# Kernel tuning notes

Measured on AMD Instinct MI355X. Metric: run time of the kernel, lower is better.

The kernel has to match this reference:

```python
import jax, jax.numpy as jnp
import numpy as np

# ---- Cl(3,0) Cayley table; blade order [1, e1,e2,e3, e12,e13,e23, e123] ----
def _build_cayley():
    blades = [0b000, 0b001, 0b010, 0b100, 0b011, 0b101, 0b110, 0b111]
    pos = {b: i for i, b in enumerate(blades)}
    def sign(a, b):
        s, a = 0, a >> 1
        while a:
            s += bin(a & b).count('1')
            a >>= 1
        return -1.0 if s & 1 else 1.0
    C = np.zeros((8, 8, 8), np.float32)
    for i, a in enumerate(blades):
        for k, b in enumerate(blades):
            C[i, pos[a ^ b], k] = sign(a, b)  # e_a * e_b -> sign * e_(a^b), metric all +1
    return jnp.asarray(C)

CAYLEY = _build_cayley()
EPS = 1e-6
SEQ = 25      # num_nodes (5) + num_edges (20)
HEADS = 8

def _expand_grades(w):
    # [..., 4] (per-grade) -> [..., 8] (per-blade), grade dims 1,3,3,1
    return jnp.concatenate([w[..., 0:1],
                            jnp.repeat(w[..., 1:2], 3, -1),
                            jnp.repeat(w[..., 2:3], 3, -1),
                            w[..., 3:4]], axis=-1)

def mv_linear(x, w, b):
    # x [N, in, 8], w [out, in, 4], b [out]; bias only on scalar blade
    y = jnp.einsum('nmi,omi->noi', x, _expand_grades(w))
    return y.at[..., 0].add(b)

def mv_layernorm(x, a):
    n = jnp.linalg.norm(x, axis=-1, keepdims=True)   # [N, c, 1] multivector norm
    n = jnp.mean(n, axis=1, keepdims=True) + EPS     # mean over channels -> [N, 1, 1]
    return a[None, :, None] * x / n

def mv_silu(x, a, b):
    # invariants: scalar component + squared grade magnitudes (mag2)
    inv = jnp.stack([x[..., 0],
                     jnp.sum(x[..., 1:4] ** 2, -1),
                     jnp.sum(x[..., 4:7] ** 2, -1),
                     x[..., 7] ** 2], axis=-1)       # [N, c, 4]
    return _expand_grades(jax.nn.sigmoid(a * inv + b)) * x

def geometric_product(a, b):
    return jnp.einsum('nci,ijk,nck->ncj', a, CAYLEY, b)


def setup_inputs() -> dict:
    key = jax.random.key(0)
    ks = iter(jax.random.split(key, 40))
    D, B = 128, 1024
    N = B * SEQ
    s = 0.05
    rn = lambda *sh: jax.random.normal(next(ks), sh, jnp.float32) * s
    return dict(
        src=jax.random.normal(next(ks), (N, D, 8), jnp.float32),
        ln1_a=jnp.ones(D, jnp.float32), ln2_a=jnp.ones(D, jnp.float32), ln3_a=jnp.ones(D, jnp.float32),
        wq=rn(D, D, 4), bq=jnp.zeros(D, jnp.float32),
        wk=rn(D, D, 4), bk=jnp.zeros(D, jnp.float32),
        wv=rn(D, D, 4), bv=jnp.zeros(D, jnp.float32),
        wo=rn(D, D, 4), bo=jnp.zeros(D, jnp.float32),
        gw1=rn(2 * D, D, 4), gb1=jnp.zeros(2 * D, jnp.float32),
        gw2=rn(2 * D, D, 4), gb2=jnp.zeros(2 * D, jnp.float32),
        gw3=rn(D, 2 * D, 4), gb3=jnp.zeros(D, jnp.float32),
        gna=jnp.ones(D, jnp.float32),
        mw1=rn(2 * D, D, 4), mb1=jnp.zeros(2 * D, jnp.float32),
        sa=jnp.ones((2 * D, 4), jnp.float32), sb=jnp.zeros((2 * D, 4), jnp.float32),
        mw2=rn(D, 2 * D, 4), mb2=jnp.zeros(D, jnp.float32),
    )


def reference(src, ln1_a, ln2_a, ln3_a, wq, bq, wk, bk, wv, bv, wo, bo,
              gw1, gb1, gw2, gb2, gw3, gb3, gna,
              mw1, mb1, sa, sb, mw2, mb2):
    N, D, _ = src.shape
    B, dh = N // SEQ, D // HEADS

    def attention(x):
        q = mv_linear(x, wq, bq).reshape(B, SEQ, HEADS, dh, 8)
        k = mv_linear(x, wk, bk).reshape(B, SEQ, HEADS, dh, 8)
        v = mv_linear(x, wv, bv).reshape(B, SEQ, HEADS, dh, 8)
        scores = jnp.einsum('bshdi,bthdi->bhst', q, k) / np.float32(np.sqrt(dh * 8))
        p = jax.nn.softmax(scores, axis=-1)
        o = jnp.einsum('bhst,bthdi->bshdi', p, v).reshape(N, D, 8)
        return mv_linear(o, wo, bo)

    # pre-norm attention + residual
    x = src + attention(mv_layernorm(src, ln1_a))
    x = mv_layernorm(x, ln2_a)
    # GP_Layer: two grade-wise linears -> geometric product -> linear -> norm
    xl = mv_linear(x, gw1, gb1)
    xr = mv_linear(x, gw2, gb2)
    g = mv_layernorm(mv_linear(geometric_product(xl, xr), gw3, gb3), gna)
    x = x + g
    x = mv_layernorm(x, ln3_a)
    # gated MLP: MVLinear -> MVSiLU -> MVLinear
    ff = mv_linear(mv_silu(mv_linear(x, mw1, mb1), sa, sb), mw2, mb2)
    return x + ff
```

## Files before the change

kernel.cpp:

```cpp
#include <hip/hip_runtime.h>
#include <hip/hip_bf16.h>
#include <math.h>

#define NROWS 25600
#define SEQL  25
#define EPSV  1e-6f

typedef __hip_bfloat16 bf16;
typedef __attribute__((ext_vector_type(4))) float f32x4;
typedef __attribute__((ext_vector_type(8))) short bf16x8;
typedef __attribute__((ext_vector_type(4))) short s16x4;
typedef unsigned int u32;

#define GLD16(gp_, lp_) __builtin_amdgcn_global_load_lds( \
    (const __attribute__((address_space(1))) u32*)(gp_), \
    (__attribute__((address_space(3))) u32*)(lp_), 16, 0, 0)

__device__ __forceinline__ float b2f(short s) {
  return __uint_as_float(((u32)(unsigned short)s) << 16);
}
__device__ __forceinline__ short f2b(float f) {
  __hip_bfloat16 h = __float2bfloat16(f);
  return *reinterpret_cast<short*>(&h);
}

__device__ __forceinline__ void gprod(const float* a, const float* b, float* r) {
  const int M[8] = {0,1,2,4,3,5,6,7};
  const int P[8] = {0,1,2,4,3,5,6,7};
#pragma unroll
  for (int i = 0; i < 8; ++i) {
    const int ma = M[i];
#pragma unroll
    for (int k = 0; k < 8; ++k) {
      const int mb = M[k];
      int par = 0;
      for (int t = ma >> 1; t; t >>= 1) par += __popc(t & mb);
      const float s = (par & 1) ? -1.f : 1.f;
      r[P[ma ^ mb]] += s * a[i] * b[k];
    }
  }
}

template<int KT, int ON>
__global__ __launch_bounds__(256) void gemm_kernel(
    const bf16* __restrict__ A, const bf16* __restrict__ W,
    const float* __restrict__ bias, const float* __restrict__ invnm,
    bf16* __restrict__ Y)
{
  __shared__ __align__(16) short As[128 * 128];
  __shared__ __align__(16) short Bs[128 * 128];
  const int tid  = threadIdx.x;
  const int lane = tid & 63;
  const int wid  = tid >> 6;
  const int pl   = blockIdx.z;
  const int g    = (pl == 0) ? 0 : ((pl < 4) ? 1 : ((pl < 7) ? 2 : 3));
  const size_t n0 = (size_t)blockIdx.x * 128;
  const int c0    = blockIdx.y * 128;
  const bf16* Ab = A + (size_t)pl * NROWS * KT + n0 * KT;
  const bf16* Wb = W + ((size_t)g * ON + c0) * KT;

  f32x4 acc[4][4];
#pragma unroll
  for (int i = 0; i < 4; ++i)
#pragma unroll
    for (int j = 0; j < 4; ++j) acc[i][j] = (f32x4){0.f, 0.f, 0.f, 0.f};

  const int wm = (wid & 1) * 64;
  const int wn = (wid >> 1) * 64;
  const int lg  = lane >> 4;
  const int c8  = lane & 15;
  const int l15 = lane & 15;

  constexpr int NC = KT / 128;
#pragma unroll
  for (int kc = 0; kc < NC; ++kc) {
#pragma unroll
    for (int j = 0; j < 8; ++j) {
      const int row = wid * 32 + j * 4 + lg;
      const int sw = (c8 ^ (row & 7)) * 8;
      const bf16* ga = Ab + (size_t)row * KT + kc * 128 + sw;
      const bf16* gb = Wb + (size_t)row * KT + kc * 128 + sw;
      GLD16(ga, &As[wid * 4096 + j * 512]);
      GLD16(gb, &Bs[wid * 4096 + j * 512]);
    }
    __syncthreads();
#pragma unroll
    for (int ks = 0; ks < 4; ++ks) {
      bf16x8 af[4], bg[4];
#pragma unroll
      for (int i = 0; i < 4; ++i) {
        const int rA = wm + i * 16 + l15;
        const int rB = wn + i * 16 + l15;
        af[i] = *(const bf16x8*)&As[rA * 128 + (((ks * 4 + lg) ^ (rA & 7)) * 8)];
        bg[i] = *(const bf16x8*)&Bs[rB * 128 + (((ks * 4 + lg) ^ (rB & 7)) * 8)];
      }
#pragma unroll
      for (int mi = 0; mi < 4; ++mi)
#pragma unroll
        for (int ni = 0; ni < 4; ++ni)
          acc[mi][ni] = __builtin_amdgcn_mfma_f32_16x16x32_bf16(af[mi], bg[ni], acc[mi][ni], 0, 0, 0);
    }
    if (kc + 1 < NC) __syncthreads();
  }

  const int cr = (lane >> 4) * 4;
  const int cc = lane & 15;
  bf16* Yb = Y + (size_t)pl * NROWS * ON;
#pragma unroll
  for (int mi = 0; mi < 4; ++mi) {
#pragma unroll
    for (int j = 0; j < 4; ++j) {
      const size_t n = n0 + wm + mi * 16 + cr + j;
      const float sc = invnm ? invnm[n] : 1.f;
#pragma unroll
      for (int ni = 0; ni < 4; ++ni) {
        const int colg = c0 + wn + ni * 16 + cc;
        float v = acc[mi][ni][j] * sc;
        if (pl == 0) v += bias[colg];
        Yb[n * ON + colg] = __float2bfloat16(v);
      }
    }
  }
}

__global__ __launch_bounds__(256) void wprep_all_kernel(
    const float* wq, const float* wk, const float* wv, const float* wo,
    const float* gw1, const float* gw2, const float* gw3,
    const float* mw1, const float* mw2,
    const float* ln1, const float* ln2, const float* ln3,
    bf16* WQ, bf16* WK, bf16* WV, bf16* WO,
    bf16* WG1, bf16* WG2, bf16* WG3, bf16* WM1, bf16* WM2)
{
  const int gid = blockIdx.x * 256 + threadIdx.x;
  const float* w; const float* ln; bf16* out; int K; int idx; int sz;
  if      (gid <  16384) { w=wq;  ln=ln1;     out=WQ;  K=128; idx=gid;          sz=16384; }
  else if (gid <  32768) { w=wk;  ln=ln1;     out=WK;  K=128; idx=gid-16384;    sz=16384; }
  else if (gid <  49152) { w=wv;  ln=ln1;     out=WV;  K=128; idx=gid-32768;    sz=16384; }
  else if (gid <  65536) { w=wo;  ln=nullptr; out=WO;  K=128; idx=gid-49152;    sz=16384; }
  else if (gid <  98304) { w=gw1; ln=ln2;     out=WG1; K=128; idx=gid-65536;    sz=32768; }
  else if (gid < 131072) { w=gw2; ln=ln2;     out=WG2; K=128; idx=gid-98304;    sz=32768; }
  else if (gid < 163840) { w=gw3; ln=nullptr; out=WG3; K=256; idx=gid-131072;   sz=32768; }
  else if (gid < 196608) { w=mw1; ln=ln3;     out=WM1; K=128; idx=gid-163840;   sz=32768; }
  else                   { w=mw2; ln=nullptr; out=WM2; K=256; idx=gid-196608;   sz=32768; }
  const int k = idx % K;
  const float s = ln ? ln[k] : 1.f;
  const float4 wv4 = *(const float4*)(w + (size_t)idx * 4);
  out[0 * sz + idx] = __float2bfloat16(wv4.x * s);
  out[1 * sz + idx] = __float2bfloat16(wv4.y * s);
  out[2 * sz + idx] = __float2bfloat16(wv4.z * s);
  out[3 * sz + idx] = __float2bfloat16(wv4.w * s);
}

__global__ __launch_bounds__(256) void repack_kernel(
    const float* __restrict__ src, bf16* __restrict__ Xp, float* __restrict__ nminv)
{
  const int tid = threadIdx.x;
  const size_t base = ((size_t)blockIdx.x * 256 + tid) * 4;
  const size_t P = (size_t)NROWS * 128;
  float v[4][8];
  const float4* sp = (const float4*)(src + base * 8);
  float part = 0.f;
#pragma unroll
  for (int e = 0; e < 4; ++e) {
    const float4 a = sp[e * 2], b = sp[e * 2 + 1];
    v[e][0]=a.x; v[e][1]=a.y; v[e][2]=a.z; v[e][3]=a.w;
    v[e][4]=b.x; v[e][5]=b.y; v[e][6]=b.z; v[e][7]=b.w;
    float ss = 0.f;
#pragma unroll
    for (int p = 0; p < 8; ++p) ss += v[e][p] * v[e][p];
    part += sqrtf(ss);
  }
#pragma unroll
  for (int p = 0; p < 8; ++p) {
    s16x4 o;
#pragma unroll
    for (int e = 0; e < 4; ++e) o[e] = f2b(v[e][p]);
    *(s16x4*)(Xp + p * P + base) = o;
  }
#pragma unroll
  for (int off = 1; off < 32; off <<= 1) part += __shfl_xor(part, off);
  if ((tid & 31) == 0) nminv[base >> 7] = 1.f / (part / 128.f + EPSV);
}

__global__ __launch_bounds__(256) void attn_kernel(
    bf16* __restrict__ Q, const bf16* __restrict__ K, const bf16* __restrict__ V)
{
  __shared__ float Pld[4][32 * 36];
  const int tid  = threadIdx.x;
  const int lane = tid & 63;
  const int wid  = tid >> 6;
  const int job  = blockIdx.x * 4 + wid;
  const int b    = job >> 3;
  const int h    = job & 7;
  const size_t PS = (size_t)NROWS * 128;
  const int rowbase = b * SEQL;
  const int l15 = lane & 15;
  const int lg  = lane >> 4;

  f32x4 acc[2][2];
#pragma unroll
  for (int si = 0; si < 2; ++si)
#pragma unroll
    for (int ti = 0; ti < 2; ++ti) acc[si][ti] = (f32x4){0.f,0.f,0.f,0.f};

#pragma unroll
  for (int ks = 0; ks < 4; ++ks) {
    const int f = ks * 32 + lg * 8;
    const int p = f >> 4, d = f & 15;
    bf16x8 aq[2], bk[2];
#pragma unroll
    for (int si = 0; si < 2; ++si) {
      int s = si * 16 + l15; if (s > 24) s = 24;
      aq[si] = *(const bf16x8*)(Q + (size_t)p * PS + (size_t)(rowbase + s) * 128 + h * 16 + d);
    }
#pragma unroll
    for (int ti = 0; ti < 2; ++ti) {
      int t = ti * 16 + l15; if (t > 24) t = 24;
      bk[ti] = *(const bf16x8*)(K + (size_t)p * PS + (size_t)(rowbase + t) * 128 + h * 16 + d);
    }
#pragma unroll
    for (int si = 0; si < 2; ++si)
#pragma unroll
      for (int ti = 0; ti < 2; ++ti)
        acc[si][ti] = __builtin_amdgcn_mfma_f32_16x16x32_bf16(aq[si], bk[ti], acc[si][ti], 0, 0, 0);
  }

  const float scale = 0.08838834764831845f;
  float pv[2][2][4];
#pragma unroll
  for (int si = 0; si < 2; ++si)
#pragma unroll
    for (int ti = 0; ti < 2; ++ti)
#pragma unroll
      for (int r = 0; r < 4; ++r) {
        float v = acc[si][ti][r] * scale;
        if (ti * 16 + l15 > 24) v = -1e30f;
        pv[si][ti][r] = v;
      }
#pragma unroll
  for (int si = 0; si < 2; ++si)
#pragma unroll
    for (int r = 0; r < 4; ++r) {
      float m = fmaxf(pv[si][0][r], pv[si][1][r]);
#pragma unroll
      for (int off = 1; off < 16; off <<= 1) m = fmaxf(m, __shfl_xor(m, off));
      const float e0 = __expf(pv[si][0][r] - m);
      const float e1 = __expf(pv[si][1][r] - m);
      float sum = e0 + e1;
#pragma unroll
      for (int off = 1; off < 16; off <<= 1) sum += __shfl_xor(sum, off);
      const float inv = 1.f / sum;
      pv[si][0][r] = e0 * inv;
      pv[si][1][r] = e1 * inv;
    }

  float* Pw = &Pld[wid][0];
#pragma unroll
  for (int si = 0; si < 2; ++si)
#pragma unroll
    for (int ti = 0; ti < 2; ++ti)
#pragma unroll
      for (int r = 0; r < 4; ++r)
        Pw[(si * 16 + lg * 4 + r) * 36 + ti * 16 + l15] = pv[si][ti][r];
  __syncthreads();

  const int p2 = lane >> 3;
  const int d2 = (lane & 7) * 2;
  const bf16* vb = V + (size_t)p2 * PS + (size_t)rowbase * 128 + h * 16 + d2;
  float vlo[32], vhi[32];
#pragma unroll
  for (int t = 0; t < SEQL; ++t) {
    const __hip_bfloat162 vv = *(const __hip_bfloat162*)(vb + (size_t)t * 128);
    vlo[t] = __bfloat162float(vv.x);
    vhi[t] = __bfloat162float(vv.y);
  }
#pragma unroll
  for (int t = SEQL; t < 32; ++t) { vlo[t] = 0.f; vhi[t] = 0.f; }

  bf16* ob = Q + (size_t)p2 * PS + (size_t)rowbase * 128 + h * 16 + d2;
  for (int s = 0; s < SEQL; ++s) {
    const float4* pr = reinterpret_cast<const float4*>(&Pld[wid][s * 36]);
    float a0 = 0.f, a1 = 0.f;
#pragma unroll
    for (int t4 = 0; t4 < 8; ++t4) {
      const float4 pq = pr[t4];
      a0 += pq.x * vlo[t4*4+0] + pq.y * vlo[t4*4+1] + pq.z * vlo[t4*4+2] + pq.w * vlo[t4*4+3];
      a1 += pq.x * vhi[t4*4+0] + pq.y * vhi[t4*4+1] + pq.z * vhi[t4*4+2] + pq.w * vhi[t4*4+3];
    }
    __hip_bfloat162 o2;
    o2.x = __float2bfloat16(a0);
    o2.y = __float2bfloat16(a1);
    *(__hip_bfloat162*)(ob + (size_t)s * 128) = o2;
  }
}

__global__ __launch_bounds__(256) void xres_kernel(
    const float* __restrict__ src, const bf16* __restrict__ AO,
    bf16* __restrict__ X, float* __restrict__ nminv)
{
  const int tid = threadIdx.x;
  const size_t base = ((size_t)blockIdx.x * 256 + tid) * 4;
  const size_t P = (size_t)NROWS * 128;
  float v[4][8];
  const float4* sp = (const float4*)(src + base * 8);
#pragma unroll
  for (int e = 0; e < 4; ++e) {
    const float4 a = sp[e * 2], b = sp[e * 2 + 1];
    v[e][0]=a.x; v[e][1]=a.y; v[e][2]=a.z; v[e][3]=a.w;
    v[e][4]=b.x; v[e][5]=b.y; v[e][6]=b.z; v[e][7]=b.w;
  }
  float part = 0.f;
  float ss[4] = {0.f, 0.f, 0.f, 0.f};
#pragma unroll
  for (int p = 0; p < 8; ++p) {
    const s16x4 av = *(const s16x4*)(AO + p * P + base);
    s16x4 o;
#pragma unroll
    for (int e = 0; e < 4; ++e) {
      v[e][p] += b2f(av[e]);
      o[e] = f2b(v[e][p]);
      ss[e] += v[e][p] * v[e][p];
    }
    *(s16x4*)(X + p * P + base) = o;
  }
#pragma unroll
  for (int e = 0; e < 4; ++e) part += sqrtf(ss[e]);
#pragma unroll
  for (int off = 1; off < 32; off <<= 1) part += __shfl_xor(part, off);
  if ((tid & 31) == 0) nminv[base >> 7] = 1.f / (part / 128.f + EPSV);
}

__global__ __launch_bounds__(256) void gp_kernel(
    bf16* __restrict__ XL, const bf16* __restrict__ XR)
{
  const size_t base = ((size_t)blockIdx.x * 256 + threadIdx.x) * 4;
  const size_t P = (size_t)NROWS * 256;
  s16x4 av[8], bv[8], rv[8];
#pragma unroll
  for (int p = 0; p < 8; ++p) {
    av[p] = *(const s16x4*)(XL + p * P + base);
    bv[p] = *(const s16x4*)(XR + p * P + base);
  }
#pragma unroll
  for (int e = 0; e < 4; ++e) {
    float a[8], b[8], r[8] = {0.f,0.f,0.f,0.f,0.f,0.f,0.f,0.f};
#pragma unroll
    for (int p = 0; p < 8; ++p) { a[p] = b2f(av[p][e]); b[p] = b2f(bv[p][e]); }
    gprod(a, b, r);
#pragma unroll
    for (int p = 0; p < 8; ++p) rv[p][e] = f2b(r[p]);
  }
#pragma unroll
  for (int p = 0; p < 8; ++p) *(s16x4*)(XL + p * P + base) = rv[p];
}

__global__ __launch_bounds__(256) void combine_kernel(
    bf16* __restrict__ X, const bf16* __restrict__ Gl,
    const float* __restrict__ ln2a, const float* __restrict__ gna,
    const float* __restrict__ nm2inv, float* __restrict__ nm4inv)
{
  const int tid = threadIdx.x;
  const size_t base = ((size_t)blockIdx.x * 256 + tid) * 4;
  const size_t P = (size_t)NROWS * 128;
  const size_t n = base >> 7;
  const int c = (int)(base & 127);

  float gv[4][8];
  float ssg[4] = {0.f,0.f,0.f,0.f};
#pragma unroll
  for (int p = 0; p < 8; ++p) {
    const s16x4 g4 = *(const s16x4*)(Gl + p * P + base);
#pragma unroll
    for (int e = 0; e < 4; ++e) { gv[e][p] = b2f(g4[e]); ssg[e] += gv[e][p] * gv[e][p]; }
  }
  float partg = sqrtf(ssg[0]) + sqrtf(ssg[1]) + sqrtf(ssg[2]) + sqrtf(ssg[3]);
#pragma unroll
  for (int off = 1; off < 32; off <<= 1) partg += __shfl_xor(partg, off);
  const float invg = 1.f / (partg / 128.f + EPSV);

  const float n2 = nm2inv[n];
  float s2[4], sg[4];
#pragma unroll
  for (int e = 0; e < 4; ++e) { s2[e] = ln2a[c + e] * n2; sg[e] = gna[c + e] * invg; }

  float ss[4] = {0.f,0.f,0.f,0.f};
#pragma unroll
  for (int p = 0; p < 8; ++p) {
    const s16x4 x4 = *(const s16x4*)(X + p * P + base);
    s16x4 o;
#pragma unroll
    for (int e = 0; e < 4; ++e) {
      const float v = s2[e] * b2f(x4[e]) + sg[e] * gv[e][p];
      o[e] = f2b(v);
      ss[e] += v * v;
    }
    *(s16x4*)(X + p * P + base) = o;
  }
  float part = sqrtf(ss[0]) + sqrtf(ss[1]) + sqrtf(ss[2]) + sqrtf(ss[3]);
#pragma unroll
  for (int off = 1; off < 32; off <<= 1) part += __shfl_xor(part, off);
  if ((tid & 31) == 0) nm4inv[n] = 1.f / (part / 128.f + EPSV);
}

__global__ __launch_bounds__(256) void silu_kernel(
    bf16* __restrict__ H, const float* __restrict__ sa, const float* __restrict__ sb)
{
  const size_t base = ((size_t)blockIdx.x * 256 + threadIdx.x) * 4;
  const int c = (int)(base & 255);
  const size_t P = (size_t)NROWS * 256;
  s16x4 hv[8];
#pragma unroll
  for (int p = 0; p < 8; ++p) hv[p] = *(const s16x4*)(H + p * P + base);
#pragma unroll
  for (int e = 0; e < 4; ++e) {
    float v[8];
#pragma unroll
    for (int p = 0; p < 8; ++p) v[p] = b2f(hv[p][e]);
    const float i0 = v[0];
    const float i1 = v[1]*v[1] + v[2]*v[2] + v[3]*v[3];
    const float i2 = v[4]*v[4] + v[5]*v[5] + v[6]*v[6];
    const float i3 = v[7]*v[7];
    const int cc = c + e;
    const float g0 = 1.f / (1.f + __expf(-(sa[cc*4+0]*i0 + sb[cc*4+0])));
    const float g1 = 1.f / (1.f + __expf(-(sa[cc*4+1]*i1 + sb[cc*4+1])));
    const float g2 = 1.f / (1.f + __expf(-(sa[cc*4+2]*i2 + sb[cc*4+2])));
    const float g3 = 1.f / (1.f + __expf(-(sa[cc*4+3]*i3 + sb[cc*4+3])));
    v[0]*=g0; v[1]*=g1; v[2]*=g1; v[3]*=g1; v[4]*=g2; v[5]*=g2; v[6]*=g2; v[7]*=g3;
#pragma unroll
    for (int p = 0; p < 8; ++p) hv[p][e] = f2b(v[p]);
  }
#pragma unroll
  for (int p = 0; p < 8; ++p) *(s16x4*)(H + p * P + base) = hv[p];
}

__global__ __launch_bounds__(256) void final_kernel(
    const bf16* __restrict__ X3, const bf16* __restrict__ FF,
    const float* __restrict__ ln3a, const float* __restrict__ nm4inv,
    float* __restrict__ out)
{
  const size_t base = ((size_t)blockIdx.x * 256 + threadIdx.x) * 4;
  const int c = (int)(base & 127);
  const size_t n = base >> 7;
  const size_t P = (size_t)NROWS * 128;
  const float nm = nm4inv[n];
  float o[4][8];
#pragma unroll
  for (int p = 0; p < 8; ++p) {
    const s16x4 x4 = *(const s16x4*)(X3 + p * P + base);
    const s16x4 f4 = *(const s16x4*)(FF + p * P + base);
#pragma unroll
    for (int e = 0; e < 4; ++e)
      o[e][p] = ln3a[c + e] * nm * b2f(x4[e]) + b2f(f4[e]);
  }
  float4* op = (float4*)(out + base * 8);
#pragma unroll
  for (int e = 0; e < 4; ++e) {
    float4 lo, hi;
    lo.x=o[e][0]; lo.y=o[e][1]; lo.z=o[e][2]; lo.w=o[e][3];
    hi.x=o[e][4]; hi.y=o[e][5]; hi.z=o[e][6]; hi.w=o[e][7];
    op[e * 2] = lo;
    op[e * 2 + 1] = hi;
  }
}

extern "C" void kernel_launch(void* const* d_in, const int* in_sizes, int n_in,
                              void* d_out, int out_size, void* d_ws, size_t ws_size,
                              hipStream_t stream) {
  (void)in_sizes; (void)n_in; (void)out_size; (void)ws_size;
  const float* src   = (const float*)d_in[0];
  const float* ln1_a = (const float*)d_in[1];
  const float* ln2_a = (const float*)d_in[2];
  const float* ln3_a = (const float*)d_in[3];
  const float* wq = (const float*)d_in[4];  const float* bq = (const float*)d_in[5];
  const float* wk = (const float*)d_in[6];  const float* bk = (const float*)d_in[7];
  const float* wv = (const float*)d_in[8];  const float* bv = (const float*)d_in[9];
  const float* wo = (const float*)d_in[10]; const float* bo = (const float*)d_in[11];
  const float* gw1 = (const float*)d_in[12]; const float* gb1 = (const float*)d_in[13];
  const float* gw2 = (const float*)d_in[14]; const float* gb2 = (const float*)d_in[15];
  const float* gw3 = (const float*)d_in[16]; const float* gb3 = (const float*)d_in[17];
  const float* gna = (const float*)d_in[18];
  const float* mw1 = (const float*)d_in[19]; const float* mb1 = (const float*)d_in[20];
  const float* sa  = (const float*)d_in[21]; const float* sb  = (const float*)d_in[22];
  const float* mw2 = (const float*)d_in[23]; const float* mb2 = (const float*)d_in[24];

  const size_t P128 = (size_t)NROWS * 128;
  char* ws = (char*)d_ws;
  bf16* R1 = (bf16*)ws;
  bf16* R2 = (bf16*)(ws + 104857600);
  bf16* WQ = (bf16*)(ws + 157286400);
  bf16* WK = WQ + 65536;
  bf16* WV = WK + 65536;
  bf16* WO = WV + 65536;
  bf16* WG1 = WO + 65536;
  bf16* WG2 = WG1 + 131072;
  bf16* WG3 = WG2 + 131072;
  bf16* WM1 = WG3 + 131072;
  bf16* WM2 = WM1 + 131072;
  float* nm1 = (float*)(ws + 159121408);
  float* nm2 = nm1 + NROWS;
  float* nm4 = nm2 + NROWS;

  bf16* Dd = (bf16*)d_out;
  bf16* Xp = R2;
  bf16* Kp = R1;
  bf16* Vp = R1 + P128;

  wprep_all_kernel<<<896, 256, 0, stream>>>(
      wq, wk, wv, wo, gw1, gw2, gw3, mw1, mw2,
      ln1_a, ln2_a, ln3_a,
      WQ, WK, WV, WO, WG1, WG2, WG3, WM1, WM2);

  repack_kernel<<<3200, 256, 0, stream>>>(src, Xp, nm1);

  dim3 g128(NROWS / 128, 1, 8), g256(NROWS / 128, 2, 8);
  gemm_kernel<128, 128><<<g128, 256, 0, stream>>>(Xp, WQ, bq, nm1, Dd);
  gemm_kernel<128, 128><<<g128, 256, 0, stream>>>(Xp, WK, bk, nm1, Kp);
  gemm_kernel<128, 128><<<g128, 256, 0, stream>>>(Xp, WV, bv, nm1, Vp);

  attn_kernel<<<2048, 256, 0, stream>>>(Dd, Kp, Vp);

  gemm_kernel<128, 128><<<g128, 256, 0, stream>>>(Dd, WO, bo, nullptr, Kp);

  xres_kernel<<<3200, 256, 0, stream>>>(src, Kp, Xp, nm2);

  gemm_kernel<128, 256><<<g256, 256, 0, stream>>>(Xp, WG1, gb1, nm2, Dd);
  gemm_kernel<128, 256><<<g256, 256, 0, stream>>>(Xp, WG2, gb2, nm2, R1);

  gp_kernel<<<6400, 256, 0, stream>>>(Dd, R1);

  gemm_kernel<256, 128><<<g128, 256, 0, stream>>>(Dd, WG3, gb3, nullptr, Kp);

  combine_kernel<<<3200, 256, 0, stream>>>(Xp, Kp, ln2_a, gna, nm2, nm4);

  gemm_kernel<128, 256><<<g256, 256, 0, stream>>>(Xp, WM1, mb1, nm4, Dd);

  silu_kernel<<<6400, 256, 0, stream>>>(Dd, sa, sb);

  gemm_kernel<256, 128><<<g128, 256, 0, stream>>>(Dd, WM2, mb2, nullptr, Vp);

  final_kernel<<<3200, 256, 0, stream>>>(Xp, Vp, ln3_a, nm4, (float*)d_out);
}
```

Measured before the change: 620.6 us.

## Fuse layernorm repack, QKV projections and attention into one per-batch kernel

Replaces the repack kernel, three QKV GEMMs and the attention kernel with a single kernel per batch element. It loads src into LDS, computes the layernorm scale, projects Q/K/V per head with MFMA from LDS, and runs softmax and PV with MFMA. This removes the bf16 write and re-read of Q, K and V through global memory and cuts four launches. In exchange each block needs a large amount of LDS, which limits occupancy. Weights are reloaded per head, and the projection work per block is serialized across only four waves.

```diff
diff --git a/kernel.cpp b/kernel.cpp
--- a/kernel.cpp
+++ b/kernel.cpp
@@ -128,169 +128,238 @@
     const float* gw1, const float* gw2, const float* gw3,
     const float* mw1, const float* mw2,
     const float* ln1, const float* ln2, const float* ln3,
-    bf16* WQ, bf16* WK, bf16* WV, bf16* WO,
-    bf16* WG1, bf16* WG2, bf16* WG3, bf16* WM1, bf16* WM2)
+    bf16* WQKV, bf16* WO, bf16* WG1, bf16* WG2, bf16* WG3, bf16* WM1, bf16* WM2)
 {
   const int gid = blockIdx.x * 256 + threadIdx.x;
-  const float* w; const float* ln; bf16* out; int K; int idx; int sz;
-  if      (gid <  16384) { w=wq;  ln=ln1;     out=WQ;  K=128; idx=gid;          sz=16384; }
-  else if (gid <  32768) { w=wk;  ln=ln1;     out=WK;  K=128; idx=gid-16384;    sz=16384; }
-  else if (gid <  49152) { w=wv;  ln=ln1;     out=WV;  K=128; idx=gid-32768;    sz=16384; }
-  else if (gid <  65536) { w=wo;  ln=nullptr; out=WO;  K=128; idx=gid-49152;    sz=16384; }
-  else if (gid <  98304) { w=gw1; ln=ln2;     out=WG1; K=128; idx=gid-65536;    sz=32768; }
-  else if (gid < 131072) { w=gw2; ln=ln2;     out=WG2; K=128; idx=gid-98304;    sz=32768; }
-  else if (gid < 163840) { w=gw3; ln=nullptr; out=WG3; K=256; idx=gid-131072;   sz=32768; }
-  else if (gid < 196608) { w=mw1; ln=ln3;     out=WM1; K=128; idx=gid-163840;   sz=32768; }
-  else                   { w=mw2; ln=nullptr; out=WM2; K=256; idx=gid-196608;   sz=32768; }
+  const float* w; const float* ln; bf16* out; int K; int idx; int planeSz; int rowOfs;
+  if      (gid <  16384) { w=wq;  ln=ln1;     out=WQKV; K=128; idx=gid;        planeSz=49152; rowOfs=0;   }
+  else if (gid <  32768) { w=wk;  ln=ln1;     out=WQKV; K=128; idx=gid-16384;  planeSz=49152; rowOfs=128; }
+  else if (gid <  49152) { w=wv;  ln=ln1;     out=WQKV; K=128; idx=gid-32768;  planeSz=49152; rowOfs=256; }
+  else if (gid <  65536) { w=wo;  ln=nullptr; out=WO;   K=128; idx=gid-49152;  planeSz=16384; rowOfs=0;   }
+  else if (gid <  98304) { w=gw1; ln=ln2;     out=WG1;  K=128; idx=gid-65536;  planeSz=32768; rowOfs=0;   }
+  else if (gid < 131072) { w=gw2; ln=ln2;     out=WG2;  K=128; idx=gid-98304;  planeSz=32768; rowOfs=0;   }
+  else if (gid < 163840) { w=gw3; ln=nullptr; out=WG3;  K=256; idx=gid-131072; planeSz=32768; rowOfs=0;   }
+  else if (gid < 196608) { w=mw1; ln=ln3;     out=WM1;  K=128; idx=gid-163840; planeSz=32768; rowOfs=0;   }
+  else                   { w=mw2; ln=nullptr; out=WM2;  K=256; idx=gid-196608; planeSz=32768; rowOfs=0;   }
   const int k = idx % K;
   const float s = ln ? ln[k] : 1.f;
   const float4 wv4 = *(const float4*)(w + (size_t)idx * 4);
-  out[0 * sz + idx] = __float2bfloat16(wv4.x * s);
-  out[1 * sz + idx] = __float2bfloat16(wv4.y * s);
-  out[2 * sz + idx] = __float2bfloat16(wv4.z * s);
-  out[3 * sz + idx] = __float2bfloat16(wv4.w * s);
-}
-
-__global__ __launch_bounds__(256) void repack_kernel(
-    const float* __restrict__ src, bf16* __restrict__ Xp, float* __restrict__ nminv)
-{
-  const int tid = threadIdx.x;
-  const size_t base = ((size_t)blockIdx.x * 256 + tid) * 4;
-  const size_t P = (size_t)NROWS * 128;
-  float v[4][8];
-  const float4* sp = (const float4*)(src + base * 8);
-  float part = 0.f;
-#pragma unroll
-  for (int e = 0; e < 4; ++e) {
-    const float4 a = sp[e * 2], b = sp[e * 2 + 1];
-    v[e][0]=a.x; v[e][1]=a.y; v[e][2]=a.z; v[e][3]=a.w;
-    v[e][4]=b.x; v[e][5]=b.y; v[e][6]=b.z; v[e][7]=b.w;
-    float ss = 0.f;
-#pragma unroll
-    for (int p = 0; p < 8; ++p) ss += v[e][p] * v[e][p];
-    part += sqrtf(ss);
-  }
-#pragma unroll
-  for (int p = 0; p < 8; ++p) {
-    s16x4 o;
-#pragma unroll
-    for (int e = 0; e < 4; ++e) o[e] = f2b(v[e][p]);
-    *(s16x4*)(Xp + p * P + base) = o;
-  }
-#pragma unroll
-  for (int off = 1; off < 32; off <<= 1) part += __shfl_xor(part, off);
-  if ((tid & 31) == 0) nminv[base >> 7] = 1.f / (part / 128.f + EPSV);
-}
-
-__global__ __launch_bounds__(256) void attn_kernel(
-    bf16* __restrict__ Q, const bf16* __restrict__ K, const bf16* __restrict__ V)
-{
-  __shared__ float Pld[4][32 * 36];
+  bf16* dst = out + (size_t)rowOfs * K + idx;
+  dst[0 * planeSz] = __float2bfloat16(wv4.x * s);
+  dst[1 * planeSz] = __float2bfloat16(wv4.y * s);
+  dst[2 * planeSz] = __float2bfloat16(wv4.z * s);
+  dst[3 * planeSz] = __float2bfloat16(wv4.w * s);
+}
+
+__global__ __launch_bounds__(256) void attn_mega_kernel(
+    const float* __restrict__ src, const bf16* __restrict__ WQKV,
+    const float* __restrict__ bq, const float* __restrict__ bk,
+    const float* __restrict__ bv, bf16* __restrict__ O)
+{
+  __shared__ __align__(16) short Xs[8 * 25 * 128];
+  __shared__ __align__(16) short QKs[4][2][32 * 128];
+  __shared__ __align__(16) short Ps[4][32 * 32];
+  __shared__ float redN[32];
+  __shared__ float invnS[32];
+
   const int tid  = threadIdx.x;
   const int lane = tid & 63;
   const int wid  = tid >> 6;
-  const int job  = blockIdx.x * 4 + wid;
-  const int b    = job >> 3;
-  const int h    = job & 7;
+  const int l15  = lane & 15;
+  const int lg   = lane >> 4;
+  const int b    = blockIdx.x;
+  const int N0   = b * SEQL;
   const size_t PS = (size_t)NROWS * 128;
-  const int rowbase = b * SEQL;
-  const int l15 = lane & 15;
-  const int lg  = lane >> 4;
-
-  f32x4 acc[2][2];
+
+  if (tid < 32) redN[tid] = 0.f;
+  __syncthreads();
+
+  for (int i = 0; i < 13; ++i) {
+    const int q = tid + i * 256;
+    if (q < SEQL * 128) {
+      const int n = q >> 7;
+      const int c = q & 127;
+      const float* sp = src + ((size_t)(N0 + n) * 128 + c) * 8;
+      const float4 a = *(const float4*)sp;
+      const float4 bb = *(const float4*)(sp + 4);
+      float v[8] = {a.x, a.y, a.z, a.w, bb.x, bb.y, bb.z, bb.w};
+      float ss = 0.f;
+#pragma unroll
+      for (int p = 0; p < 8; ++p) ss += v[p] * v[p];
+      float nrm = sqrtf(ss);
+      const int colbase = (((c >> 3) ^ (n & 7)) * 8) + (c & 7);
+#pragma unroll
+      for (int p = 0; p < 8; ++p) Xs[p * 3200 + n * 128 + colbase] = f2b(v[p]);
+#pragma unroll
+      for (int off = 1; off < 64; off <<= 1) nrm += __shfl_xor(nrm, off);
+      if (lane == 0) atomicAdd(&redN[n], nrm);
+    }
+  }
+  __syncthreads();
+  if (tid < 32) invnS[tid] = (tid < SEQL) ? 1.f / (redN[tid] / 128.f + EPSV) : 0.f;
+  __syncthreads();
+
+  float inz[8];
 #pragma unroll
   for (int si = 0; si < 2; ++si)
 #pragma unroll
-    for (int ti = 0; ti < 2; ++ti) acc[si][ti] = (f32x4){0.f,0.f,0.f,0.f};
-
-#pragma unroll
-  for (int ks = 0; ks < 4; ++ks) {
-    const int f = ks * 32 + lg * 8;
-    const int p = f >> 4, d = f & 15;
-    bf16x8 aq[2], bk[2];
-#pragma unroll
-    for (int si = 0; si < 2; ++si) {
-      int s = si * 16 + l15; if (s > 24) s = 24;
-      aq[si] = *(const bf16x8*)(Q + (size_t)p * PS + (size_t)(rowbase + s) * 128 + h * 16 + d);
-    }
-#pragma unroll
-    for (int ti = 0; ti < 2; ++ti) {
-      int t = ti * 16 + l15; if (t > 24) t = 24;
-      bk[ti] = *(const bf16x8*)(K + (size_t)p * PS + (size_t)(rowbase + t) * 128 + h * 16 + d);
-    }
+    for (int j = 0; j < 4; ++j) inz[si * 4 + j] = invnS[si * 16 + lg * 4 + j];
+  const float inzT0 = invnS[l15];
+  const float inzT1 = invnS[16 + l15];
+
+  short* Qb = &QKs[wid][0][0];
+  short* Kb = &QKs[wid][1][0];
+  short* Pb = &Ps[wid][0];
+  const int r0c = l15;
+  const int r1c = (16 + l15 > 24) ? 24 : (16 + l15);
+
+  for (int hh = 0; hh < 2; ++hh) {
+    const int h = wid * 2 + hh;
+
+#pragma unroll
+    for (int mat = 0; mat < 2; ++mat) {
+      short* Ob = mat ? Kb : Qb;
+      const float bia = (mat ? bk : bq)[h * 16 + l15];
+      for (int p = 0; p < 8; ++p) {
+        const int g = (p == 0) ? 0 : ((p < 4) ? 1 : ((p < 7) ? 2 : 3));
+        const bf16* Wr = WQKV + ((size_t)g * 384 + mat * 128 + h * 16 + l15) * 128;
+        f32x4 a0 = (f32x4){0.f,0.f,0.f,0.f}, a1 = (f32x4){0.f,0.f,0.f,0.f};
+#pragma unroll
+        for (int ks = 0; ks < 4; ++ks) {
+          const bf16x8 wf = *(const bf16x8*)(Wr + ks * 32 + lg * 8);
+          const int c16 = ks * 4 + lg;
+          const bf16x8 x0 = *(const bf16x8*)&Xs[p * 3200 + r0c * 128 + ((c16 ^ (r0c & 7)) * 8)];
+          const bf16x8 x1 = *(const bf16x8*)&Xs[p * 3200 + r1c * 128 + ((c16 ^ (r1c & 7)) * 8)];
+          a0 = __builtin_amdgcn_mfma_f32_16x16x32_bf16(x0, wf, a0, 0, 0, 0);
+          a1 = __builtin_amdgcn_mfma_f32_16x16x32_bf16(x1, wf, a1, 0, 0, 0);
+        }
+        const int fch = p * 2 + (l15 >> 3);
+        const int fo  = l15 & 7;
+#pragma unroll
+        for (int j = 0; j < 4; ++j) {
+          const int na = lg * 4 + j;
+          const int nb = 16 + lg * 4 + j;
+          const float v0 = a0[j] * inz[j]     + ((p == 0) ? bia : 0.f);
+          const float v1 = a1[j] * inz[4 + j] + ((p == 0) ? bia : 0.f);
+          Ob[na * 128 + ((fch ^ (na & 7)) * 8) + fo] = f2b(v0);
+          Ob[nb * 128 + ((fch ^ (nb & 7)) * 8) + fo] = f2b(v1);
+        }
+      }
+    }
+
+    f32x4 sacc[2][2];
 #pragma unroll
     for (int si = 0; si < 2; ++si)
 #pragma unroll
+      for (int ti = 0; ti < 2; ++ti) sacc[si][ti] = (f32x4){0.f,0.f,0.f,0.f};
+#pragma unroll
+    for (int ks = 0; ks < 4; ++ks) {
+      const int c16 = ks * 4 + lg;
+      const int ra = l15, rb = 16 + l15;
+      const bf16x8 qa0 = *(const bf16x8*)&Qb[ra * 128 + ((c16 ^ (ra & 7)) * 8)];
+      const bf16x8 qa1 = *(const bf16x8*)&Qb[rb * 128 + ((c16 ^ (rb & 7)) * 8)];
+      const bf16x8 kb0 = *(const bf16x8*)&Kb[ra * 128 + ((c16 ^ (ra & 7)) * 8)];
+      const bf16x8 kb1 = *(const bf16x8*)&Kb[rb * 128 + ((c16 ^ (rb & 7)) * 8)];
+      sacc[0][0] = __builtin_amdgcn_mfma_f32_16x16x32_bf16(qa0, kb0, sacc[0][0], 0, 0, 0);
+      sacc[0][1] = __builtin_amdgcn_mfma_f32_16x16x32_bf16(qa0, kb1, sacc[0][1], 0, 0, 0);
+      sacc[1][0] = __builtin_amdgcn_mfma_f32_16x16x32_bf16(qa1, kb0, sacc[1][0], 0, 0, 0);
+      sacc[1][1] = __builtin_amdgcn_mfma_f32_16x16x32_bf16(qa1, kb1, sacc[1][1], 0, 0, 0);
+    }
+
+    const float scale = 0.08838834764831845f;
+    float pv[2][2][4];
+#pragma unroll
+    for (int si = 0; si < 2; ++si)
+#pragma unroll
       for (int ti = 0; ti < 2; ++ti)
-        acc[si][ti] = __builtin_amdgcn_mfma_f32_16x16x32_bf16(aq[si], bk[ti], acc[si][ti], 0, 0, 0);
-  }
-
-  const float scale = 0.08838834764831845f;
-  float pv[2][2][4];
-#pragma unroll
-  for (int si = 0; si < 2; ++si)
-#pragma unroll
-    for (int ti = 0; ti < 2; ++ti)
+#pragma unroll
+        for (int r = 0; r < 4; ++r) {
+          float v = sacc[si][ti][r] * scale;
+          if (ti * 16 + l15 > 24) v = -1e30f;
+          pv[si][ti][r] = v;
+        }
+#pragma unroll
+    for (int si = 0; si < 2; ++si)
 #pragma unroll
       for (int r = 0; r < 4; ++r) {
-        float v = acc[si][ti][r] * scale;
-        if (ti * 16 + l15 > 24) v = -1e30f;
-        pv[si][ti][r] = v;
+        float m = fmaxf(pv[si][0][r], pv[si][1][r]);
+#pragma unroll
+        for (int off = 1; off < 16; off <<= 1) m = fmaxf(m, __shfl_xor(m, off));
+        const float e0 = __expf(pv[si][0][r] - m);
+        const float e1 = __expf(pv[si][1][r] - m);
+        float sum = e0 + e1;
+#pragma unroll
+        for (int off = 1; off < 16; off <<= 1) sum += __shfl_xor(sum, off);
+        const float inv = 1.f / sum;
+        pv[si][0][r] = e0 * inv;
+        pv[si][1][r] = e1 * inv;
       }
-#pragma unroll
-  for (int si = 0; si < 2; ++si)
-#pragma unroll
-    for (int r = 0; r < 4; ++r) {
-      float m = fmaxf(pv[si][0][r], pv[si][1][r]);
-#pragma unroll
-      for (int off = 1; off < 16; off <<= 1) m = fmaxf(m, __shfl_xor(m, off));
-      const float e0 = __expf(pv[si][0][r] - m);
-      const float e1 = __expf(pv[si][1][r] - m);
-      float sum = e0 + e1;
-#pragma unroll
-      for (int off = 1; off < 16; off <<= 1) sum += __shfl_xor(sum, off);
-      const float inv = 1.f / sum;
-      pv[si][0][r] = e0 * inv;
-      pv[si][1][r] = e1 * inv;
-    }
-
-  float* Pw = &Pld[wid][0];
-#pragma unroll
-  for (int si = 0; si < 2; ++si)
-#pragma unroll
-    for (int ti = 0; ti < 2; ++ti)
-#pragma unroll
-      for (int r = 0; r < 4; ++r)
-        Pw[(si * 16 + lg * 4 + r) * 36 + ti * 16 + l15] = pv[si][ti][r];
-  __syncthreads();
-
-  const int p2 = lane >> 3;
-  const int d2 = (lane & 7) * 2;
-  const bf16* vb = V + (size_t)p2 * PS + (size_t)rowbase * 128 + h * 16 + d2;
-  float vlo[32], vhi[32];
-#pragma unroll
-  for (int t = 0; t < SEQL; ++t) {
-    const __hip_bfloat162 vv = *(const __hip_bfloat162*)(vb + (size_t)t * 128);
-    vlo[t] = __bfloat162float(vv.x);
-    vhi[t] = __bfloat162float(vv.y);
-  }
-#pragma unroll
-  for (int t = SEQL; t < 32; ++t) { vlo[t] = 0.f; vhi[t] = 0.f; }
-
-  bf16* ob = Q + (size_t)p2 * PS + (size_t)rowbase * 128 + h * 16 + d2;
-  for (int s = 0; s < SEQL; ++s) {
-    const float4* pr = reinterpret_cast<const float4*>(&Pld[wid][s * 36]);
-    float a0 = 0.f, a1 = 0.f;
-#pragma unroll
-    for (int t4 = 0; t4 < 8; ++t4) {
-      const float4 pq = pr[t4];
-      a0 += pq.x * vlo[t4*4+0] + pq.y * vlo[t4*4+1] + pq.z * vlo[t4*4+2] + pq.w * vlo[t4*4+3];
-      a1 += pq.x * vhi[t4*4+0] + pq.y * vhi[t4*4+1] + pq.z * vhi[t4*4+2] + pq.w * vhi[t4*4+3];
-    }
-    __hip_bfloat162 o2;
-    o2.x = __float2bfloat16(a0);
-    o2.y = __float2bfloat16(a1);
-    *(__hip_bfloat162*)(ob + (size_t)s * 128) = o2;
+
+#pragma unroll
+    for (int si = 0; si < 2; ++si)
+#pragma unroll
+      for (int ti = 0; ti < 2; ++ti)
+#pragma unroll
+        for (int r = 0; r < 4; ++r) {
+          const int n = si * 16 + lg * 4 + r;
+          const int t = ti * 16 + l15;
+          Pb[n * 32 + (((t >> 3) ^ (n & 3)) * 8) + (t & 7)] = f2b(pv[si][ti][r]);
+        }
+
+    short* Vt = Qb;
+    float bvj[4];
+#pragma unroll
+    for (int j = 0; j < 4; ++j) bvj[j] = bv[h * 16 + lg * 4 + j];
+    for (int p = 0; p < 8; ++p) {
+      const int g = (p == 0) ? 0 : ((p < 4) ? 1 : ((p < 7) ? 2 : 3));
+      const bf16* Wr = WQKV + ((size_t)g * 384 + 256 + h * 16 + l15) * 128;
+      f32x4 v0 = (f32x4){0.f,0.f,0.f,0.f}, v1 = (f32x4){0.f,0.f,0.f,0.f};
+#pragma unroll
+      for (int ks = 0; ks < 4; ++ks) {
+        const bf16x8 wf = *(const bf16x8*)(Wr + ks * 32 + lg * 8);
+        const int c16 = ks * 4 + lg;
+        const bf16x8 x0 = *(const bf16x8*)&Xs[p * 3200 + r0c * 128 + ((c16 ^ (r0c & 7)) * 8)];
+        const bf16x8 x1 = *(const bf16x8*)&Xs[p * 3200 + r1c * 128 + ((c16 ^ (r1c & 7)) * 8)];
+        v0 = __builtin_amdgcn_mfma_f32_16x16x32_bf16(wf, x0, v0, 0, 0, 0);
+        v1 = __builtin_amdgcn_mfma_f32_16x16x32_bf16(wf, x1, v1, 0, 0, 0);
+      }
+#pragma unroll
+      for (int j = 0; j < 4; ++j) {
+        const int f = p * 16 + lg * 4 + j;
+        const float vv0 = v0[j] * inzT0 + ((p == 0) ? bvj[j] : 0.f);
+        const float vv1 = v1[j] * inzT1 + ((p == 0) ? bvj[j] : 0.f);
+        const int t0 = l15, t1 = 16 + l15;
+        Vt[f * 32 + (((t0 >> 3) ^ (f & 3)) * 8) + (t0 & 7)] = f2b(vv0);
+        Vt[f * 32 + (((t1 >> 3) ^ (f & 3)) * 8) + (t1 & 7)] = f2b(vv1);
+      }
+    }
+
+    const bf16x8 pa0 = *(const bf16x8*)&Pb[l15 * 32 + ((lg ^ (l15 & 3)) * 8)];
+    const bf16x8 pa1 = *(const bf16x8*)&Pb[(16 + l15) * 32 + ((lg ^ ((16 + l15) & 3)) * 8)];
+    f32x4 oacc[2][8];
+#pragma unroll
+    for (int si = 0; si < 2; ++si)
+#pragma unroll
+      for (int fi = 0; fi < 8; ++fi) oacc[si][fi] = (f32x4){0.f,0.f,0.f,0.f};
+#pragma unroll
+    for (int fi = 0; fi < 8; ++fi) {
+      const int f = fi * 16 + l15;
+      const bf16x8 vb = *(const bf16x8*)&Vt[f * 32 + ((lg ^ (f & 3)) * 8)];
+      oacc[0][fi] = __builtin_amdgcn_mfma_f32_16x16x32_bf16(pa0, vb, oacc[0][fi], 0, 0, 0);
+      oacc[1][fi] = __builtin_amdgcn_mfma_f32_16x16x32_bf16(pa1, vb, oacc[1][fi], 0, 0, 0);
+    }
+
+#pragma unroll
+    for (int si = 0; si < 2; ++si)
+#pragma unroll
+      for (int fi = 0; fi < 8; ++fi)
+#pragma unroll
+        for (int j = 0; j < 4; ++j) {
+          const int n = si * 16 + lg * 4 + j;
+          if (n < SEQL)
+            O[(size_t)fi * PS + (size_t)(N0 + n) * 128 + h * 16 + l15] =
+                __float2bfloat16(oacc[si][fi][j]);
+        }
   }
 }
 
@@ -483,60 +552,47 @@
   const float* sa  = (const float*)d_in[21]; const float* sb  = (const float*)d_in[22];
   const float* mw2 = (const float*)d_in[23]; const float* mb2 = (const float*)d_in[24];
 
-  const size_t P128 = (size_t)NROWS * 128;
   char* ws = (char*)d_ws;
   bf16* R1 = (bf16*)ws;
   bf16* R2 = (bf16*)(ws + 104857600);
-  bf16* WQ = (bf16*)(ws + 157286400);
-  bf16* WK = WQ + 65536;
-  bf16* WV = WK + 65536;
-  bf16* WO = WV + 65536;
-  bf16* WG1 = WO + 65536;
-  bf16* WG2 = WG1 + 131072;
-  bf16* WG3 = WG2 + 131072;
-  bf16* WM1 = WG3 + 131072;
-  bf16* WM2 = WM1 + 131072;
-  float* nm1 = (float*)(ws + 159121408);
-  float* nm2 = nm1 + NROWS;
+  bf16* WQKV = (bf16*)(ws + 157286400);
+  bf16* WO  = WQKV + 196608;
+  bf16* WG1 = WO   + 65536;
+  bf16* WG2 = WG1  + 131072;
+  bf16* WG3 = WG2  + 131072;
+  bf16* WM1 = WG3  + 131072;
+  bf16* WM2 = WM1  + 131072;
+  float* nm2 = (float*)(ws + 159252480);
   float* nm4 = nm2 + NROWS;
 
   bf16* Dd = (bf16*)d_out;
-  bf16* Xp = R2;
-  bf16* Kp = R1;
-  bf16* Vp = R1 + P128;
 
   wprep_all_kernel<<<896, 256, 0, stream>>>(
-      wq, wk, wv, wo, gw1, gw2, gw3, mw1, mw2,
-      ln1_a, ln2_a, ln3_a,
-      WQ, WK, WV, WO, WG1, WG2, WG3, WM1, WM2);
-
-  repack_kernel<<<3200, 256, 0, stream>>>(src, Xp, nm1);
+      wq, wk, wv, wo, gw1, gw2, gw3, mw1, mw2, ln1_a, ln2_a, ln3_a,
+      WQKV, WO, WG1, WG2, WG3, WM1, WM2);
+
+  attn_mega_kernel<<<1024, 256, 0, stream>>>(src, WQKV, bq, bk, bv, R2);
 
   dim3 g128(NROWS / 128, 1, 8), g256(NROWS / 128, 2, 8);
-  gemm_kernel<128, 128><<<g128, 256, 0, stream>>>(Xp, WQ, bq, nm1, Dd);
-  gemm_kernel<128, 128><<<g128, 256, 0, stream>>>(Xp, WK, bk, nm1, Kp);
-  gemm_kernel<128, 128><<<g128, 256, 0, stream>>>(Xp, WV, bv, nm1, Vp);
-
-  attn_kernel<<<2048, 256, 0, stream>>>(Dd, Kp, Vp);
-
-  gemm_kernel<128, 128><<<g128, 256, 0, stream>>>(Dd, WO, bo, nullptr, Kp);
-
-  xres_kernel<<<3200, 256, 0, stream>>>(src, Kp, Xp, nm2);
-
-  gemm_kernel<128, 256><<<g256, 256, 0, stream>>>(Xp, WG1, gb1, nm2, Dd);
-  gemm_kernel<128, 256><<<g256, 256, 0, stream>>>(Xp, WG2, gb2, nm2, R1);
+
+  gemm_kernel<128, 128><<<g128, 256, 0, stream>>>(R2, WO, bo, nullptr, R1);
+
+  xres_kernel<<<3200, 256, 0, stream>>>(src, R1, R2, nm2);
+
+  gemm_kernel<128, 256><<<g256, 256, 0, stream>>>(R2, WG1, gb1, nm2, Dd);
+  gemm_kernel<128, 256><<<g256, 256, 0, stream>>>(R2, WG2, gb2, nm2, R1);
 
   gp_kernel<<<6400, 256, 0, stream>>>(Dd, R1);
 
-  gemm_kernel<256, 128><<<g128, 256, 0, stream>>>(Dd, WG3, gb3, nullptr, Kp);
-
-  combine_kernel<<<3200, 256, 0, stream>>>(Xp, Kp, ln2_a, gna, nm2, nm4);
-
-  gemm_kernel<128, 256><<<g256, 256, 0, stream>>>(Xp, WM1, mb1, nm4, Dd);
+  gemm_kernel<256, 128><<<g128, 256, 0, stream>>>(Dd, WG3, gb3, nullptr, R1);
+
+  combine_kernel<<<3200, 256, 0, stream>>>(R2, R1, ln2_a, gna, nm2, nm4);
+
+  gemm_kernel<128, 256><<<g256, 256, 0, stream>>>(R2, WM1, mb1, nm4, Dd);
 
   silu_kernel<<<6400, 256, 0, stream>>>(Dd, sa, sb);
 
-  gemm_kernel<256, 128><<<g128, 256, 0, stream>>>(Dd, WM2, mb2, nullptr, Vp);
-
-  final_kernel<<<3200, 256, 0, stream>>>(Xp, Vp, ln3_a, nm4, (float*)d_out);
-}
+  gemm_kernel<256, 128><<<g128, 256, 0, stream>>>(Dd, WM2, mb2, nullptr, R1);
+
+  final_kernel<<<3200, 256, 0, stream>>>(R2, R1, ln3_a, nm4, (float*)d_out);
+}
```

New measurement: 664.6 us. 7.1% more time.
